# Kernel optimization log

Hardware: AMD Instinct MI355X
Metric: run time of the kernel (lower is better)

## Reference

```python
import jax, jax.numpy as jnp
import numpy as np

B, S, T, C, H = 16, 64, 4096, 512, 8
D = C // H
NEG = jnp.float32(-1e30)


def setup_inputs() -> dict:
    key = jax.random.key(0)
    ks = jax.random.split(key, 12)
    x = jax.random.normal(ks[0], (1, C, 1), dtype=jnp.float32)
    eh = jax.random.normal(ks[1], (B, C, T), dtype=jnp.float32)
    # ragged shot boundaries -> fixed (B, S) start/end arrays, end > start
    bounds = jnp.sort(jax.random.randint(ks[2], (B, S + 1), 0, T), axis=-1)
    shot_starts = bounds[:, :-1].astype(jnp.int32)
    shot_ends = jnp.maximum(bounds[:, 1:], shot_starts + 1).astype(jnp.int32)
    sc = 1.0 / np.sqrt(C)
    Wq = jax.random.normal(ks[3], (C, C), dtype=jnp.float32) * sc
    bq = jnp.zeros((C,), dtype=jnp.float32)
    Wk = jax.random.normal(ks[4], (C, C), dtype=jnp.float32) * sc
    bk = jnp.zeros((C,), dtype=jnp.float32)
    Wv = jax.random.normal(ks[5], (C, C), dtype=jnp.float32) * sc
    bv = jnp.zeros((C,), dtype=jnp.float32)
    Wp = jax.random.normal(ks[6], (C, C), dtype=jnp.float32) * sc
    bp = jnp.zeros((C,), dtype=jnp.float32)
    return {"x": x, "encoder_hidden_states": eh, "shot_starts": shot_starts,
            "shot_ends": shot_ends, "Wq": Wq, "bq": bq, "Wk": Wk, "bk": bk,
            "Wv": Wv, "bv": bv, "Wp": Wp, "bp": bp}


def reference(x, encoder_hidden_states, shot_starts, shot_ends,
              Wq, bq, Wk, bk, Wv, bv, Wp, bp):
    scale = 1.0 / np.sqrt(D)
    # 1x1 conv == pointwise matmul over channels
    q = (Wq @ x[0] + bq[:, None])            # (C, 1)
    k = jnp.einsum('oc,bct->bot', Wk, encoder_hidden_states) + bk[None, :, None]
    v = jnp.einsum('oc,bct->bot', Wv, encoder_hidden_states) + bv[None, :, None]
    qh = q.reshape(H, D) * scale             # (H, D) single query per head
    kh = k.reshape(B, H, D, T)               # (B, H, D, T)
    vh = v.reshape(B, H, D, T).transpose(0, 1, 3, 2)  # (B, H, T, D)
    att = jnp.einsum('hd,bhdt->bht', qh, kh)          # (B, H, T)
    pos = jnp.arange(T)
    seg = (pos[None, None, :] >= shot_starts[:, :, None]) & \
          (pos[None, None, :] < shot_ends[:, :, None])  # (B, S, T)
    logits = jnp.where(seg[:, :, None, :], att[:, None, :, :], NEG)  # (B,S,H,T)
    p = jax.nn.softmax(logits, axis=-1)
    out = jnp.einsum('bsht,bhtd->bshd', p, vh)        # (B, S, H, D)
    out = out.reshape(B * S, C)
    out = out @ Wp.T + bp                              # proj (1x1 conv)
    return out[:, :, None]                             # (B*S, C, 1)
```

## Files before the change

### kernel.cpp

```cpp
#include <hip/hip_runtime.h>
#include <cstdint>
#include <cstddef>

#define B_ 16
#define S_ 64
#define T_ 4096
#define C_ 512
#define H_ 8

#define WS_QKT     0
#define WS_QB      4096
#define WS_ATT     8192
#define WS_WSUM    532480
#define WS_ATTNOUT 4726784

__global__ void k_prep(const float* __restrict__ x, const float* __restrict__ Wq,
                       const float* __restrict__ bq, const float* __restrict__ Wk,
                       const float* __restrict__ bk, float* __restrict__ qkT,
                       float* __restrict__ qb) {
  __shared__ float xs[C_];
  __shared__ float part[4][64];
  __shared__ float qh[64];
  int tid = threadIdx.x;
  int h = blockIdx.x;
  xs[tid] = x[tid];
  xs[tid + 256] = x[tid + 256];
  __syncthreads();
  int d = tid & 63, pp = tid >> 6;
  const float* wrow = Wq + (size_t)(h * 64 + d) * C_ + pp * 128;
  const float* xp = xs + pp * 128;
  float s = 0.f;
#pragma unroll 4
  for (int c = 0; c < 128; ++c) s += wrow[c] * xp[c];
  part[pp][d] = s;
  __syncthreads();
  if (tid < 64) {
    float qv = part[0][tid] + part[1][tid] + part[2][tid] + part[3][tid] +
               bq[h * 64 + tid];
    qh[tid] = qv * 0.125f;
  }
  __syncthreads();
  if (tid == 0) {
    float sb = 0.f;
    for (int dd = 0; dd < 64; ++dd) sb += qh[dd] * bk[h * 64 + dd];
    qb[h] = sb;
  }
  for (int c = tid; c < C_; c += 256) {
    float s2 = 0.f;
#pragma unroll 8
    for (int dd = 0; dd < 64; ++dd)
      s2 += qh[dd] * Wk[(size_t)(h * 64 + dd) * C_ + c];
    qkT[c * 8 + h] = s2;
  }
}

__global__ __launch_bounds__(256, 4) void k_att(
    const float* __restrict__ eh, const float* __restrict__ qkT,
    const float* __restrict__ qb, float* __restrict__ att) {
  __shared__ float qks[C_ * 8];
  __shared__ float part[4 * 8 * 64];
  int tid = threadIdx.x;
  int tl = tid & 63, cg = tid >> 6;
  int b = blockIdx.y;
  int t0 = blockIdx.x * 64;
#pragma unroll
  for (int i = 0; i < 16; ++i) qks[tid + i * 256] = qkT[tid + i * 256];
  __syncthreads();
  const float* ehp = eh + ((size_t)b * C_ + (size_t)cg * 128) * T_ + t0 + tl;
  float acc[8];
#pragma unroll
  for (int h = 0; h < 8; ++h) acc[h] = 0.f;
#pragma unroll 4
  for (int j = 0; j < 128; ++j) {
    float e = ehp[(size_t)j * T_];
    const float4 q0 = *(const float4*)&qks[(cg * 128 + j) * 8];
    const float4 q1 = *(const float4*)&qks[(cg * 128 + j) * 8 + 4];
    acc[0] += q0.x * e; acc[1] += q0.y * e; acc[2] += q0.z * e; acc[3] += q0.w * e;
    acc[4] += q1.x * e; acc[5] += q1.y * e; acc[6] += q1.z * e; acc[7] += q1.w * e;
  }
#pragma unroll
  for (int h = 0; h < 8; ++h) part[(cg * 8 + h) * 64 + tl] = acc[h];
  __syncthreads();
#pragma unroll
  for (int i = 0; i < 2; ++i) {
    int idx = tid + i * 256;
    int h = idx >> 6, tt = idx & 63;
    float v = part[(0 * 8 + h) * 64 + tt] + part[(1 * 8 + h) * 64 + tt] +
              part[(2 * 8 + h) * 64 + tt] + part[(3 * 8 + h) * 64 + tt] + qb[h];
    att[((size_t)b * H_ + h) * T_ + t0 + tt] = v;
  }
}

__global__ __launch_bounds__(256, 4) void k_wsum(
    const float* __restrict__ eh, const float* __restrict__ att,
    const int* __restrict__ starts, const int* __restrict__ ends,
    float* __restrict__ wsum) {
  __shared__ float pl[8 * 64];
  __shared__ float ms[8], li[8];
  int tid = threadIdx.x;
  int n = blockIdx.x;
  int b = n >> 6;
  int start = starts[n], end = ends[n];
  int h = tid >> 5, tl = tid & 31;
  const float* ah = att + ((size_t)b * H_ + h) * T_;

  float mloc = -3.0e38f;
  for (int t = start + tl; t < end; t += 32) mloc = fmaxf(mloc, ah[t]);
#pragma unroll
  for (int off = 16; off > 0; off >>= 1)
    mloc = fmaxf(mloc, __shfl_xor(mloc, off, 32));
  float lloc = 0.f;
  for (int t = start + tl; t < end; t += 32) lloc += __expf(ah[t] - mloc);
#pragma unroll
  for (int off = 16; off > 0; off >>= 1) lloc += __shfl_xor(lloc, off, 32);
  if (tl == 0) { ms[h] = mloc; li[h] = 1.f / lloc; }

  float acc0[8], acc1[8];
#pragma unroll
  for (int i = 0; i < 8; ++i) { acc0[i] = 0.f; acc1[i] = 0.f; }
  const float* e0p = eh + ((size_t)b * C_ + tid) * T_;
  const float* e1p = e0p + (size_t)256 * T_;
  __syncthreads();

  int tbeg = start & ~3;
  for (int t0 = tbeg; t0 < end; t0 += 64) {
#pragma unroll
    for (int i = 0; i < 2; ++i) {
      int idx = tid + i * 256;
      int hh = idx >> 6;
      int tt = t0 + (idx & 63);
      float pv = 0.f;
      if (tt >= start && tt < end)
        pv = __expf(att[((size_t)b * H_ + hh) * T_ + tt] - ms[hh]) * li[hh];
      pl[idx] = pv;
    }
    __syncthreads();
    int tend = (t0 + 64 < end) ? t0 + 64 : end;
    for (int t = t0; t < tend; t += 4) {
      float4 e0 = *(const float4*)(e0p + t);
      float4 e1 = *(const float4*)(e1p + t);
      int base = t - t0;
#pragma unroll
      for (int hh = 0; hh < 8; ++hh) {
        const float4 p = *(const float4*)&pl[hh * 64 + base];
        acc0[hh] += p.x * e0.x + p.y * e0.y + p.z * e0.z + p.w * e0.w;
        acc1[hh] += p.x * e1.x + p.y * e1.y + p.z * e1.z + p.w * e1.w;
      }
    }
    __syncthreads();
  }
  float* wp = wsum + (size_t)n * (H_ * C_);
#pragma unroll
  for (int hh = 0; hh < 8; ++hh) {
    wp[hh * C_ + tid] = acc0[hh];
    wp[hh * C_ + 256 + tid] = acc1[hh];
  }
}

__global__ __launch_bounds__(256, 4) void k_gemm(
    const float* __restrict__ A, long aRow, long aColPerY,
    const float* __restrict__ Bm, const float* __restrict__ bias,
    float* __restrict__ Cc) {
  __shared__ float As[32 * 36];
  __shared__ float Bs[64 * 36];
  int tid = threadIdx.x;
  int n0 = blockIdx.x * 32;
  int y = blockIdx.y;
  const float* Abase = A + (size_t)n0 * aRow + (size_t)y * aColPerY;
  const float* Bbase = Bm + (size_t)(y * 64) * C_;
  int tx = tid & 15, ty = tid >> 4;
  float acc[2][4];
#pragma unroll
  for (int a = 0; a < 2; ++a)
#pragma unroll
    for (int bb = 0; bb < 4; ++bb) acc[a][bb] = 0.f;
  for (int k0 = 0; k0 < 512; k0 += 32) {
#pragma unroll
    for (int i = 0; i < 4; ++i) {
      int idx = tid + i * 256;
      int r = idx >> 5, cc = idx & 31;
      As[r * 36 + cc] = Abase[(size_t)r * aRow + k0 + cc];
    }
#pragma unroll
    for (int i = 0; i < 8; ++i) {
      int idx = tid + i * 256;
      int r = idx >> 5, cc = idx & 31;
      Bs[r * 36 + cc] = Bbase[(size_t)r * C_ + k0 + cc];
    }
    __syncthreads();
#pragma unroll
    for (int k = 0; k < 32; k += 4) {
      const float4 a0 = *(const float4*)&As[(ty * 2 + 0) * 36 + k];
      const float4 a1 = *(const float4*)&As[(ty * 2 + 1) * 36 + k];
#pragma unroll
      for (int bb = 0; bb < 4; ++bb) {
        const float4 bv = *(const float4*)&Bs[(tx * 4 + bb) * 36 + k];
        acc[0][bb] += a0.x * bv.x + a0.y * bv.y + a0.z * bv.z + a0.w * bv.w;
        acc[1][bb] += a1.x * bv.x + a1.y * bv.y + a1.z * bv.z + a1.w * bv.w;
      }
    }
    __syncthreads();
  }
#pragma unroll
  for (int a = 0; a < 2; ++a) {
    int nn = n0 + ty * 2 + a;
    float4 o;
    o.x = acc[a][0] + bias[y * 64 + tx * 4 + 0];
    o.y = acc[a][1] + bias[y * 64 + tx * 4 + 1];
    o.z = acc[a][2] + bias[y * 64 + tx * 4 + 2];
    o.w = acc[a][3] + bias[y * 64 + tx * 4 + 3];
    *(float4*)&Cc[(size_t)nn * C_ + y * 64 + tx * 4] = o;
  }
}

extern "C" void kernel_launch(void* const* d_in, const int* in_sizes, int n_in,
                              void* d_out, int out_size, void* d_ws,
                              size_t ws_size, hipStream_t stream) {
  const float* x = (const float*)d_in[0];
  const float* eh = (const float*)d_in[1];
  const int* shot_starts = (const int*)d_in[2];
  const int* shot_ends = (const int*)d_in[3];
  const float* Wq = (const float*)d_in[4];
  const float* bq = (const float*)d_in[5];
  const float* Wk = (const float*)d_in[6];
  const float* bk = (const float*)d_in[7];
  const float* Wv = (const float*)d_in[8];
  const float* bv = (const float*)d_in[9];
  const float* Wp = (const float*)d_in[10];
  const float* bp = (const float*)d_in[11];
  float* out = (float*)d_out;

  float* ws = (float*)d_ws;
  float* qkT = ws + WS_QKT;
  float* qb = ws + WS_QB;
  float* att = ws + WS_ATT;
  float* wsum = ws + WS_WSUM;
  float* attnout = ws + WS_ATTNOUT;

  k_prep<<<8, 256, 0, stream>>>(x, Wq, bq, Wk, bk, qkT, qb);
  k_att<<<dim3(T_ / 64, B_), 256, 0, stream>>>(eh, qkT, qb, att);
  k_wsum<<<B_ * S_, 256, 0, stream>>>(eh, att, shot_starts, shot_ends, wsum);
  k_gemm<<<dim3(32, 8), 256, 0, stream>>>(wsum, (long)(H_ * C_), (long)C_, Wv,
                                          bv, attnout);
  k_gemm<<<dim3(32, 8), 256, 0, stream>>>(attnout, (long)C_, 0L, Wp, bp, out);
}
```

Before: 396.7 us.

## Split segment weighted-sum into fixed-size time chunks with atomic accumulation

Splits k_wsum so each block handles one chunk of up to 128 timesteps of a segment. A small mapping kernel builds the chunk list per batch, and a separate stats kernel computes the per-segment softmax max and inverse sum. This is meant to balance work across blocks when segment lengths are ragged, so long segments no longer serialize inside one block. The prep kernel is also split into two kernels with more parallelism. The cost is extra launches, a memset of the 16 MB wsum buffer, and atomicAdd traffic for segments that span several chunks.

```diff
diff --git a/kernel.cpp b/kernel.cpp
--- a/kernel.cpp
+++ b/kernel.cpp
@@ -10,47 +10,71 @@
 
 #define WS_QKT     0
 #define WS_QB      4096
-#define WS_ATT     8192
-#define WS_WSUM    532480
-#define WS_ATTNOUT 4726784
-
-__global__ void k_prep(const float* __restrict__ x, const float* __restrict__ Wq,
-                       const float* __restrict__ bq, const float* __restrict__ Wk,
-                       const float* __restrict__ bk, float* __restrict__ qkT,
-                       float* __restrict__ qb) {
+#define WS_QH      4104
+#define WS_MS      4616
+#define WS_LI      12808
+#define WS_CNT     21000
+#define WS_CSEG    21016
+#define WS_CIDX    23064
+#define WS_CMUL    25112
+#define WS_ATT     28672
+#define WS_WSUM    552960
+#define WS_ATTNOUT 4747264
+
+__global__ void k_prep1(const float* __restrict__ x, const float* __restrict__ Wq,
+                        const float* __restrict__ bq, float* __restrict__ qh_g) {
   __shared__ float xs[C_];
-  __shared__ float part[4][64];
-  __shared__ float qh[64];
-  int tid = threadIdx.x;
-  int h = blockIdx.x;
+  __shared__ float red[256];
+  int tid = threadIdx.x;
   xs[tid] = x[tid];
   xs[tid + 256] = x[tid + 256];
   __syncthreads();
-  int d = tid & 63, pp = tid >> 6;
-  const float* wrow = Wq + (size_t)(h * 64 + d) * C_ + pp * 128;
-  const float* xp = xs + pp * 128;
+  int r0 = blockIdx.x * 32;
+  int rl = tid >> 3, sub = tid & 7;
+  int r = r0 + rl;
+  const float* wr = Wq + (size_t)r * C_ + sub * 64;
+  const float* xp = xs + sub * 64;
   float s = 0.f;
-#pragma unroll 4
-  for (int c = 0; c < 128; ++c) s += wrow[c] * xp[c];
-  part[pp][d] = s;
-  __syncthreads();
+#pragma unroll
+  for (int i = 0; i < 64; i += 4) {
+    float4 w = *(const float4*)(wr + i);
+    s += w.x * xp[i] + w.y * xp[i + 1] + w.z * xp[i + 2] + w.w * xp[i + 3];
+  }
+  red[tid] = s;
+  __syncthreads();
+  if (sub == 0) {
+    float tot = bq[r];
+#pragma unroll
+    for (int i = 0; i < 8; ++i) tot += red[rl * 8 + i];
+    qh_g[r] = tot * 0.125f;
+  }
+}
+
+__global__ void k_prep2(const float* __restrict__ qh_g,
+                        const float* __restrict__ Wk,
+                        const float* __restrict__ bk, float* __restrict__ qkT,
+                        float* __restrict__ qb) {
+  __shared__ float qhs[64];
+  int tid = threadIdx.x;
+  int h = blockIdx.x;
+  if (tid < 64) qhs[tid] = qh_g[h * 64 + tid];
+  __syncthreads();
+  int c0 = tid, c1 = tid + 256;
+  float s0 = 0.f, s1 = 0.f;
+#pragma unroll 8
+  for (int d = 0; d < 64; ++d) {
+    const float* row = Wk + (size_t)(h * 64 + d) * C_;
+    float q = qhs[d];
+    s0 += q * row[c0];
+    s1 += q * row[c1];
+  }
+  qkT[c0 * 8 + h] = s0;
+  qkT[c1 * 8 + h] = s1;
   if (tid < 64) {
-    float qv = part[0][tid] + part[1][tid] + part[2][tid] + part[3][tid] +
-               bq[h * 64 + tid];
-    qh[tid] = qv * 0.125f;
-  }
-  __syncthreads();
-  if (tid == 0) {
-    float sb = 0.f;
-    for (int dd = 0; dd < 64; ++dd) sb += qh[dd] * bk[h * 64 + dd];
-    qb[h] = sb;
-  }
-  for (int c = tid; c < C_; c += 256) {
-    float s2 = 0.f;
-#pragma unroll 8
-    for (int dd = 0; dd < 64; ++dd)
-      s2 += qh[dd] * Wk[(size_t)(h * 64 + dd) * C_ + c];
-    qkT[c * 8 + h] = s2;
+    float w = qhs[tid] * bk[h * 64 + tid];
+#pragma unroll
+    for (int off = 32; off > 0; off >>= 1) w += __shfl_down(w, off, 64);
+    if (tid == 0) qb[h] = w;
   }
 }
 
@@ -91,19 +115,16 @@
   }
 }
 
-__global__ __launch_bounds__(256, 4) void k_wsum(
-    const float* __restrict__ eh, const float* __restrict__ att,
-    const int* __restrict__ starts, const int* __restrict__ ends,
-    float* __restrict__ wsum) {
-  __shared__ float pl[8 * 64];
-  __shared__ float ms[8], li[8];
+__global__ void k_stats(const float* __restrict__ att,
+                        const int* __restrict__ starts,
+                        const int* __restrict__ ends, float* __restrict__ ms,
+                        float* __restrict__ li) {
   int tid = threadIdx.x;
   int n = blockIdx.x;
   int b = n >> 6;
   int start = starts[n], end = ends[n];
   int h = tid >> 5, tl = tid & 31;
   const float* ah = att + ((size_t)b * H_ + h) * T_;
-
   float mloc = -3.0e38f;
   for (int t = start + tl; t < end; t += 32) mloc = fmaxf(mloc, ah[t]);
 #pragma unroll
@@ -113,47 +134,108 @@
   for (int t = start + tl; t < end; t += 32) lloc += __expf(ah[t] - mloc);
 #pragma unroll
   for (int off = 16; off > 0; off >>= 1) lloc += __shfl_xor(lloc, off, 32);
-  if (tl == 0) { ms[h] = mloc; li[h] = 1.f / lloc; }
+  if (tl == 0) { ms[n * 8 + h] = mloc; li[n * 8 + h] = 1.f / lloc; }
+}
+
+__global__ void k_map(const int* __restrict__ starts,
+                      const int* __restrict__ ends, int* __restrict__ cnt,
+                      int* __restrict__ cseg, int* __restrict__ cidx,
+                      int* __restrict__ cmul) {
+  int b = blockIdx.x;
+  int s = threadIdx.x;
+  int st = starts[b * 64 + s], en = ends[b * 64 + s];
+  int cbase = st & ~31;
+  int nch = (en - cbase + 127) >> 7;
+  int x = nch;
+#pragma unroll
+  for (int off = 1; off < 64; off <<= 1) {
+    int y = __shfl_up(x, off, 64);
+    if (s >= off) x += y;
+  }
+  int pre = x - nch;
+  for (int k = 0; k < nch; ++k) {
+    cseg[b * 128 + pre + k] = s;
+    cidx[b * 128 + pre + k] = k;
+    cmul[b * 128 + pre + k] = (nch > 1) ? 1 : 0;
+  }
+  if (s == 63) cnt[b] = x;
+}
+
+__global__ __launch_bounds__(256, 4) void k_wsum(
+    const float* __restrict__ eh, const float* __restrict__ att,
+    const float* __restrict__ ms, const float* __restrict__ li,
+    const int* __restrict__ starts, const int* __restrict__ ends,
+    const int* __restrict__ cnt, const int* __restrict__ cseg,
+    const int* __restrict__ cidx, const int* __restrict__ cmul,
+    float* __restrict__ wsum) {
+  __shared__ float pl[8 * 136];
+  int b = blockIdx.y;
+  int i = blockIdx.x;
+  if (i >= cnt[b]) return;
+  int tid = threadIdx.x;
+  int s = cseg[b * 128 + i];
+  int k = cidx[b * 128 + i];
+  int mul = cmul[b * 128 + i];
+  int n = b * 64 + s;
+  int st = starts[n], en = ends[n];
+  int cbase = st & ~31;
+  int t_lo = cbase + k * 128;
+  if (st > t_lo) t_lo = st;
+  int t_hi = cbase + (k + 1) * 128;
+  if (en < t_hi) t_hi = en;
+  int base = t_lo & ~3;
+
+  int h = tid >> 5, l32 = tid & 31;
+  float msn = ms[n * 8 + h], lin = li[n * 8 + h];
+  const float* ah = att + ((size_t)b * H_ + h) * T_;
+  for (int j = l32; j < 136; j += 32) {
+    int t = base + j;
+    float pv = 0.f;
+    if (t >= t_lo && t < t_hi) pv = __expf(ah[t] - msn) * lin;
+    pl[h * 136 + j] = pv;
+  }
+  __syncthreads();
 
   float acc0[8], acc1[8];
 #pragma unroll
-  for (int i = 0; i < 8; ++i) { acc0[i] = 0.f; acc1[i] = 0.f; }
-  const float* e0p = eh + ((size_t)b * C_ + tid) * T_;
+  for (int hh = 0; hh < 8; ++hh) { acc0[hh] = 0.f; acc1[hh] = 0.f; }
+  const float* e0p = eh + ((size_t)b * C_ + tid) * T_ + base;
   const float* e1p = e0p + (size_t)256 * T_;
-  __syncthreads();
-
-  int tbeg = start & ~3;
-  for (int t0 = tbeg; t0 < end; t0 += 64) {
-#pragma unroll
-    for (int i = 0; i < 2; ++i) {
-      int idx = tid + i * 256;
-      int hh = idx >> 6;
-      int tt = t0 + (idx & 63);
-      float pv = 0.f;
-      if (tt >= start && tt < end)
-        pv = __expf(att[((size_t)b * H_ + hh) * T_ + tt] - ms[hh]) * li[hh];
-      pl[idx] = pv;
-    }
-    __syncthreads();
-    int tend = (t0 + 64 < end) ? t0 + 64 : end;
-    for (int t = t0; t < tend; t += 4) {
-      float4 e0 = *(const float4*)(e0p + t);
-      float4 e1 = *(const float4*)(e1p + t);
-      int base = t - t0;
-#pragma unroll
-      for (int hh = 0; hh < 8; ++hh) {
-        const float4 p = *(const float4*)&pl[hh * 64 + base];
-        acc0[hh] += p.x * e0.x + p.y * e0.y + p.z * e0.z + p.w * e0.w;
-        acc1[hh] += p.x * e1.x + p.y * e1.y + p.z * e1.z + p.w * e1.w;
-      }
-    }
-    __syncthreads();
+  int jmax = t_hi - base;
+  int jv = jmax & ~3;
+#pragma unroll 2
+  for (int j = 0; j < jv; j += 4) {
+    float4 e0 = *(const float4*)(e0p + j);
+    float4 e1 = *(const float4*)(e1p + j);
+#pragma unroll
+    for (int hh = 0; hh < 8; ++hh) {
+      const float4 p = *(const float4*)&pl[hh * 136 + j];
+      acc0[hh] += p.x * e0.x + p.y * e0.y + p.z * e0.z + p.w * e0.w;
+      acc1[hh] += p.x * e1.x + p.y * e1.y + p.z * e1.z + p.w * e1.w;
+    }
+  }
+  for (int j = jv; j < jmax; ++j) {
+    float e0 = e0p[j], e1 = e1p[j];
+#pragma unroll
+    for (int hh = 0; hh < 8; ++hh) {
+      float p = pl[hh * 136 + j];
+      acc0[hh] += p * e0;
+      acc1[hh] += p * e1;
+    }
   }
   float* wp = wsum + (size_t)n * (H_ * C_);
-#pragma unroll
-  for (int hh = 0; hh < 8; ++hh) {
-    wp[hh * C_ + tid] = acc0[hh];
-    wp[hh * C_ + 256 + tid] = acc1[hh];
+  if (!mul) {
+#pragma unroll
+    for (int hh = 0; hh < 8; ++hh) {
+      wp[hh * C_ + tid] = acc0[hh];
+      wp[hh * C_ + 256 + tid] = acc1[hh];
+    }
+  } else {
+#pragma unroll
+    for (int hh = 0; hh < 8; ++hh) {
+      atomicAdd(&wp[hh * C_ + tid], acc0[hh]);
+      atomicAdd(&wp[hh * C_ + 256 + tid], acc1[hh]);
+    }
   }
 }
 
@@ -233,13 +315,26 @@
   float* ws = (float*)d_ws;
   float* qkT = ws + WS_QKT;
   float* qb = ws + WS_QB;
+  float* qh = ws + WS_QH;
+  float* ms = ws + WS_MS;
+  float* li = ws + WS_LI;
+  int* cnt = (int*)(ws + WS_CNT);
+  int* cseg = (int*)(ws + WS_CSEG);
+  int* cidx = (int*)(ws + WS_CIDX);
+  int* cmul = (int*)(ws + WS_CMUL);
   float* att = ws + WS_ATT;
   float* wsum = ws + WS_WSUM;
   float* attnout = ws + WS_ATTNOUT;
 
-  k_prep<<<8, 256, 0, stream>>>(x, Wq, bq, Wk, bk, qkT, qb);
+  hipMemsetAsync(wsum, 0, (size_t)1024 * H_ * C_ * sizeof(float), stream);
+  k_prep1<<<16, 256, 0, stream>>>(x, Wq, bq, qh);
+  k_prep2<<<8, 256, 0, stream>>>(qh, Wk, bk, qkT, qb);
   k_att<<<dim3(T_ / 64, B_), 256, 0, stream>>>(eh, qkT, qb, att);
-  k_wsum<<<B_ * S_, 256, 0, stream>>>(eh, att, shot_starts, shot_ends, wsum);
+  k_stats<<<B_ * S_, 256, 0, stream>>>(att, shot_starts, shot_ends, ms, li);
+  k_map<<<B_, 64, 0, stream>>>(shot_starts, shot_ends, cnt, cseg, cidx, cmul);
+  k_wsum<<<dim3(128, B_), 256, 0, stream>>>(eh, att, ms, li, shot_starts,
+                                            shot_ends, cnt, cseg, cidx, cmul,
+                                            wsum);
   k_gemm<<<dim3(32, 8), 256, 0, stream>>>(wsum, (long)(H_ * C_), (long)C_, Wv,
                                           bv, attnout);
   k_gemm<<<dim3(32, 8), 256, 0, stream>>>(attnout, (long)C_, 0L, Wp, bp, out);
```

Result: faster. 373.9 us (-5.8%).
